# Optimization experiments

Hardware: AMD Instinct MI355X
Metric: run time of the kernel (lower is better)

## Reference

```python
import jax, jax.numpy as jnp
import numpy as np

N_NODES = 100000
N_EDGES = 1600000
IN_C = 128
HID = 128
OUT_C = 10
N_GRAPHS = 512


def setup_inputs() -> dict:
    key = jax.random.key(0)
    ks = jax.random.split(key, 12)
    x = jax.random.normal(ks[0], (N_NODES, IN_C), dtype=jnp.float32)
    edge_index = jax.random.randint(ks[1], (2, N_EDGES), 0, N_NODES, dtype=jnp.int64)
    batch = jnp.sort(jax.random.randint(ks[2], (N_NODES,), 0, N_GRAPHS, dtype=jnp.int64))

    def lin(k, fan_in, fan_out):
        bound = 1.0 / np.sqrt(fan_in)
        return jax.random.uniform(k, (fan_in, fan_out), jnp.float32, -bound, bound)

    params = {
        # GraphConv layer i: W_rel (neighbor aggregate transform, with bias),
        # W_root (self transform, no bias) -- matches PyG GraphConv.
        "W1_rel": lin(ks[3], IN_C, HID), "b1": jnp.zeros((HID,), jnp.float32), "W1_root": lin(ks[4], IN_C, HID),
        "W2_rel": lin(ks[5], HID, HID), "b2": jnp.zeros((HID,), jnp.float32), "W2_root": lin(ks[6], HID, HID),
        "W3_rel": lin(ks[7], HID, HID), "b3": jnp.zeros((HID,), jnp.float32), "W3_root": lin(ks[8], HID, HID),
        "W_lin": lin(ks[9], HID, OUT_C), "b_lin": jnp.zeros((OUT_C,), jnp.float32),
    }
    return {"x": x, "edge_index": edge_index, "batch": batch, **params}


def _graph_conv(x, src, dst, W_rel, b, W_root):
    # PyG GraphConv with aggr='add': out_i = W_rel @ sum_{j->i} x_j + b + W_root @ x_i
    agg = jax.ops.segment_sum(x[src], dst, num_segments=x.shape[0])  # [N, d]
    return agg @ W_rel + b + x @ W_root


def reference(x, edge_index, batch,
              W1_rel, b1, W1_root,
              W2_rel, b2, W2_root,
              W3_rel, b3, W3_root,
              W_lin, b_lin):
    src, dst = edge_index[0], edge_index[1]
    h = jax.nn.relu(_graph_conv(x, src, dst, W1_rel, b1, W1_root))
    h = jax.nn.relu(_graph_conv(h, src, dst, W2_rel, b2, W2_root))
    h = _graph_conv(h, src, dst, W3_rel, b3, W3_root)
    # global mean pool over graphs
    sums = jax.ops.segment_sum(h, batch, num_segments=N_GRAPHS)             # [G, d]
    counts = jax.ops.segment_sum(jnp.ones((h.shape[0],), h.dtype), batch, num_segments=N_GRAPHS)
    pooled = sums / jnp.maximum(counts, 1.0)[:, None]
    return pooled @ W_lin + b_lin  # [G, OUT_C]
```

## Files before the change

### kernel.cpp

```cpp
#include <hip/hip_runtime.h>

static constexpr int NN = 100000;
static constexpr int NE = 1600000;
static constexpr int C  = 128;
static constexpr int OC = 10;
static constexpr int NG = 512;

static constexpr int BSH  = 9;
static constexpr int BNW  = 1 << BSH;
static constexpr int BK   = (NN + BNW - 1) / BNW;
static constexpr int BCAP = 12288;
static constexpr int EPB  = 8192;
static constexpr int ABLK = (NE + EPB - 1) / EPB;

static constexpr int TSTRIDE = 132;
static constexpr int NSPLIT = 8;

typedef unsigned short u16;
typedef __attribute__((ext_vector_type(8))) short short8;
typedef __attribute__((ext_vector_type(8))) short bf16x8;
typedef __attribute__((ext_vector_type(4))) float f32x4;

__device__ __forceinline__ float bf2f(u16 u) {
    union { float f; unsigned int u32; } v; v.u32 = ((unsigned int)u) << 16; return v.f;
}
__device__ __forceinline__ u16 f2bf(float f) {
    union { float f; unsigned int u; } v; v.f = f;
    unsigned int u = v.u;
    unsigned int r = u + 0x7FFF + ((u >> 16) & 1);
    return (u16)(r >> 16);
}

__global__ __launch_bounds__(256) void k_binA(const int* __restrict__ src,
                                              const int* __restrict__ dst,
                                              int* __restrict__ gcnt,
                                              int* __restrict__ buck) {
    __shared__ int cnt[BK];
    __shared__ int curs[BK];
    int tid = threadIdx.x;
    for (int i = tid; i < BK; i += 256) cnt[i] = 0;
    __syncthreads();
    int e0 = blockIdx.x * EPB;
    for (int i = tid; i < EPB; i += 256) {
        int e = e0 + i;
        if (e < NE) atomicAdd(&cnt[dst[e] >> BSH], 1);
    }
    __syncthreads();
    for (int i = tid; i < BK; i += 256) {
        int c = cnt[i];
        int gb = (c > 0) ? atomicAdd(&gcnt[i], c) : 0;
        curs[i] = i * BCAP + gb;
    }
    __syncthreads();
    for (int i = tid; i < EPB; i += 256) {
        int e = e0 + i;
        if (e < NE) {
            int d = dst[e];
            int b = d >> BSH;
            int p = atomicAdd(&curs[b], 1);
            if (p < (b + 1) * BCAP)
                buck[p] = (src[e] << BSH) | (d & (BNW - 1));
        }
    }
}

__global__ __launch_bounds__(256) void k_meta(const int* __restrict__ gcnt,
                                              int* __restrict__ csrbase,
                                              int* __restrict__ rp,
                                              const int* __restrict__ batch,
                                              int* __restrict__ gstart) {
    int tid = threadIdx.x;
    if (blockIdx.x == 0) {
        __shared__ int buf[256];
        int v = (tid < BK) ? gcnt[tid] : 0;
        buf[tid] = v;
        __syncthreads();
        for (int off = 1; off < 256; off <<= 1) {
            int t = (tid >= off) ? buf[tid - off] : 0;
            __syncthreads();
            buf[tid] += t;
            __syncthreads();
        }
        if (tid < BK) csrbase[tid] = buf[tid] - v;
        if (tid == 0) rp[NN] = NE;
    } else {
        int g = (blockIdx.x - 1) * 256 + tid;
        if (g > NG) return;
        int lo = 0, hi = NN;
        while (lo < hi) { int mid = (lo + hi) >> 1; if (batch[mid] < g) lo = mid + 1; else hi = mid; }
        gstart[g] = lo;
    }
}

__global__ __launch_bounds__(BNW) void k_binB(const int* __restrict__ gcnt,
                                              const int* __restrict__ csrbase,
                                              const int* __restrict__ buck,
                                              int* __restrict__ rp,
                                              int* __restrict__ csr) {
    int b = blockIdx.x;
    int tid = threadIdx.x;
    __shared__ int hist[BNW];
    __shared__ int scanbuf[BNW];
    int n = gcnt[b];
    if (n > BCAP) n = BCAP;
    int base = csrbase[b];
    const int* bb = buck + (size_t)b * BCAP;

    hist[tid] = 0;
    __syncthreads();
    for (int i = tid; i < n; i += BNW) atomicAdd(&hist[bb[i] & (BNW - 1)], 1);
    __syncthreads();

    int v = hist[tid];
    scanbuf[tid] = v;
    __syncthreads();
    for (int off = 1; off < BNW; off <<= 1) {
        int t = (tid >= off) ? scanbuf[tid - off] : 0;
        __syncthreads();
        scanbuf[tid] += t;
        __syncthreads();
    }
    int excl = scanbuf[tid] - v;
    int node = (b << BSH) + tid;
    if (node < NN) rp[node] = base + excl;
    __syncthreads();
    hist[tid] = base + excl;
    __syncthreads();
    for (int i = tid; i < n; i += BNW) {
        int en = bb[i];
        int p = atomicAdd(&hist[en & (BNW - 1)], 1);
        csr[p] = en >> BSH;
    }
}

__global__ __launch_bounds__(256) void k_prep(
    const float* __restrict__ x, u16* __restrict__ xb,
    const float* __restrict__ W1r, const float* __restrict__ W1o,
    const float* __restrict__ W2r, const float* __restrict__ W2o,
    u16* __restrict__ Bp) {
    int bid = blockIdx.x;
    if (bid < 32) {
        int layer = bid >> 4;
        const float* Wr = (layer == 0) ? W1r : W2r;
        const float* Wo = (layer == 0) ? W1o : W2o;
        u16* out = Bp + layer * 32768;
        int t = (bid & 15) * 256 + threadIdx.x;
        int lane = t & 63;
        int nfrag = (t >> 6) & 7;
        int kk = t >> 9;
        int col = nfrag * 16 + (lane & 15);
        int k0 = kk * 32 + (lane >> 4) * 8;
        u16 vals[8];
#pragma unroll
        for (int j = 0; j < 8; ++j) {
            int k = k0 + j;
            float w = (k < C) ? Wr[k * C + col] : Wo[(k - C) * C + col];
            vals[j] = f2bf(w);
        }
        *reinterpret_cast<short8*>(out + (size_t)t * 8) = *reinterpret_cast<const short8*>(vals);
    } else {
        int i = (bid - 32) * 256 + threadIdx.x;
        size_t base = (size_t)i * 8;
        if (base >= (size_t)NN * C) return;
        float4 a = *reinterpret_cast<const float4*>(x + base);
        float4 b = *reinterpret_cast<const float4*>(x + base + 4);
        u16 o[8] = { f2bf(a.x), f2bf(a.y), f2bf(a.z), f2bf(a.w),
                     f2bf(b.x), f2bf(b.y), f2bf(b.z), f2bf(b.w) };
        *reinterpret_cast<short8*>(xb + base) = *reinterpret_cast<const short8*>(o);
    }
}

__global__ __launch_bounds__(256) void k_wfold(
    const float* __restrict__ W3r, const float* __restrict__ W3o,
    const float* __restrict__ b3, const float* __restrict__ W_lin,
    const float* __restrict__ b_lin,
    float* __restrict__ Wrl, float* __restrict__ Wro, float* __restrict__ bfold) {
    int o = blockIdx.x;
    int tid = threadIdx.x;
    if (tid < 128) {
        float s = 0.0f;
#pragma unroll 8
        for (int c = 0; c < C; ++c) s += W3r[tid * C + c] * W_lin[c * OC + o];
        Wrl[tid * OC + o] = s;
    } else {
        int k = tid - 128;
        float s = 0.0f;
#pragma unroll 8
        for (int c = 0; c < C; ++c) s += W3o[k * C + c] * W_lin[c * OC + o];
        Wro[k * OC + o] = s;
    }
    if (tid == 0) {
        float s = 0.0f;
        for (int c = 0; c < C; ++c) s += b3[c] * W_lin[c * OC + o];
        bfold[o] = b_lin[o] + s;
    }
}

__global__ __launch_bounds__(256) void k_gather(const u16* __restrict__ h,
                                                const int* __restrict__ rp,
                                                const int* __restrict__ csr,
                                                u16* __restrict__ agg) {
    int t = blockIdx.x * blockDim.x + threadIdx.x;
    int node = t >> 6;
    if (node >= NN) return;
    int lane = t & 63;
    int jj = lane >> 4;
    int seg = (lane & 15) * 8;
    int beg = rp[node], end = rp[node + 1];

    float acc[8] = {};
    int j0 = beg;
    for (; j0 + 8 <= end; j0 += 8) {
        int sa = csr[j0 + jj];
        int sb = csr[j0 + 4 + jj];
        short8 va = *reinterpret_cast<const short8*>(h + (size_t)sa * C + seg);
        short8 vb = *reinterpret_cast<const short8*>(h + (size_t)sb * C + seg);
#pragma unroll
        for (int q = 0; q < 8; ++q) {
            acc[q] += bf2f((u16)va[q]);
            acc[q] += bf2f((u16)vb[q]);
        }
    }
    if (j0 < end) {
        int ja = j0 + jj;
        int jb = j0 + 4 + jj;
        if (ja < end) {
            int sa = csr[ja];
            short8 va = *reinterpret_cast<const short8*>(h + (size_t)sa * C + seg);
#pragma unroll
            for (int q = 0; q < 8; ++q) acc[q] += bf2f((u16)va[q]);
        }
        if (jb < end) {
            int sb = csr[jb];
            short8 vb = *reinterpret_cast<const short8*>(h + (size_t)sb * C + seg);
#pragma unroll
            for (int q = 0; q < 8; ++q) acc[q] += bf2f((u16)vb[q]);
        }
    }

#pragma unroll
    for (int q = 0; q < 8; ++q) {
        acc[q] += __shfl_xor(acc[q], 32);
        acc[q] += __shfl_xor(acc[q], 16);
    }
    if (lane < 16) {
        u16 o[8];
#pragma unroll
        for (int q = 0; q < 8; ++q) o[q] = f2bf(acc[q]);
        *reinterpret_cast<short8*>(agg + (size_t)node * C + seg) =
            *reinterpret_cast<const short8*>(o);
    }
}

template <bool RELU>
__global__ __launch_bounds__(256) void k_transform_mfma(
    const u16* __restrict__ agg, const u16* __restrict__ h,
    const u16* __restrict__ Bp, const float* __restrict__ bias,
    u16* __restrict__ out) {
    __shared__ u16 tile[4][16 * TSTRIDE];
    int wave = threadIdx.x >> 6;
    int lane = threadIdx.x & 63;
    int row0 = blockIdx.x * 64 + wave * 16;
    int arow = row0 + (lane & 15);
    int rclamp = arow < NN ? arow : NN - 1;
    int koff = (lane >> 4) * 8;

    f32x4 acc[8] = {};
#pragma unroll
    for (int kk = 0; kk < 8; ++kk) {
        bf16x8 a;
        if (kk < 4) {
            a = *reinterpret_cast<const bf16x8*>(agg + (size_t)rclamp * C + kk * 32 + koff);
        } else {
            a = *reinterpret_cast<const bf16x8*>(h + (size_t)rclamp * C + (kk - 4) * 32 + koff);
        }
        const u16* bp = Bp + ((size_t)kk * 8 * 64 + lane) * 8;
#pragma unroll
        for (int n = 0; n < 8; ++n) {
            bf16x8 b = *reinterpret_cast<const bf16x8*>(bp + (size_t)n * 64 * 8);
            acc[n] = __builtin_amdgcn_mfma_f32_16x16x32_bf16(a, b, acc[n], 0, 0, 0);
        }
    }

    u16* T = tile[wave];
    int colbase = lane & 15;
    int rloc = (lane >> 4) * 4;
#pragma unroll
    for (int n = 0; n < 8; ++n) {
        int col = n * 16 + colbase;
        float bb = bias[col];
#pragma unroll
        for (int r = 0; r < 4; ++r) {
            float v = acc[n][r] + bb;
            if (RELU) v = fmaxf(v, 0.0f);
            T[(rloc + r) * TSTRIDE + col] = f2bf(v);
        }
    }
    __syncthreads();

#pragma unroll
    for (int k = 0; k < 4; ++k) {
        int idx = k * 64 + lane;
        int lr = idx >> 4;
        int off = (idx & 15) * 8;
        int ro = row0 + lr;
        if (ro < NN) {
            short8 v = *reinterpret_cast<const short8*>(&T[lr * TSTRIDE + off]);
            *reinterpret_cast<short8*>(out + (size_t)ro * C + off) = v;
        }
    }
}

__global__ __launch_bounds__(256) void k_gsum(
    const u16* __restrict__ h, const int* __restrict__ rp,
    const int* __restrict__ csr, const int* __restrict__ gstart,
    float* __restrict__ partial) {
    int b = blockIdx.x;
    int g = b >> 3;
    int p = b & 7;
    int slot = threadIdx.x >> 4;
    int seg = (threadIdx.x & 15) * 8;

    int gs = gstart[g], ge = gstart[g + 1];
    int es = rp[gs], ee = rp[ge];
    int m = ee - es;
    int js = es + (int)(((long long)m * p) >> 3);
    int je = es + (int)(((long long)m * (p + 1)) >> 3);
    int nn = ge - gs;
    int is = gs + (int)(((long long)nn * p) >> 3);
    int ie = gs + (int)(((long long)nn * (p + 1)) >> 3);

    float accS[8] = {};
    int j = js + slot;
    for (; j + 16 < je; j += 32) {
        int r0 = csr[j];
        int r1 = csr[j + 16];
        short8 v0 = *reinterpret_cast<const short8*>(h + (size_t)r0 * C + seg);
        short8 v1 = *reinterpret_cast<const short8*>(h + (size_t)r1 * C + seg);
#pragma unroll
        for (int q = 0; q < 8; ++q) {
            accS[q] += bf2f((u16)v0[q]);
            accS[q] += bf2f((u16)v1[q]);
        }
    }
    if (j < je) {
        int r0 = csr[j];
        short8 v0 = *reinterpret_cast<const short8*>(h + (size_t)r0 * C + seg);
#pragma unroll
        for (int q = 0; q < 8; ++q) accS[q] += bf2f((u16)v0[q]);
    }

    float accT[8] = {};
    for (int i = is + slot; i < ie; i += 16) {
        short8 v = *reinterpret_cast<const short8*>(h + (size_t)i * C + seg);
#pragma unroll
        for (int q = 0; q < 8; ++q) accT[q] += bf2f((u16)v[q]);
    }

    __shared__ float red[16][C];
#pragma unroll
    for (int q = 0; q < 8; ++q) red[slot][seg + q] = accS[q];
    __syncthreads();
    if (threadIdx.x < C) {
        float s = 0.0f;
#pragma unroll
        for (int r = 0; r < 16; ++r) s += red[r][threadIdx.x];
        partial[(size_t)b * 256 + threadIdx.x] = s;
    }
    __syncthreads();
#pragma unroll
    for (int q = 0; q < 8; ++q) red[slot][seg + q] = accT[q];
    __syncthreads();
    if (threadIdx.x < C) {
        float s = 0.0f;
#pragma unroll
        for (int r = 0; r < 16; ++r) s += red[r][threadIdx.x];
        partial[(size_t)b * 256 + 128 + threadIdx.x] = s;
    }
}

__global__ __launch_bounds__(128) void k_gout(
    const float* __restrict__ partial, const int* __restrict__ gstart,
    const float* __restrict__ Wrl, const float* __restrict__ Wro,
    const float* __restrict__ bfold, float* __restrict__ out) {
    int g = blockIdx.x;
    int k = threadIdx.x;
    __shared__ float S[C], T[C];
    float s = 0.0f, t = 0.0f;
#pragma unroll
    for (int p = 0; p < NSPLIT; ++p) {
        s += partial[((size_t)(g * NSPLIT + p)) * 256 + k];
        t += partial[((size_t)(g * NSPLIT + p)) * 256 + 128 + k];
    }
    S[k] = s;
    T[k] = t;
    __syncthreads();
    if (k < OC) {
        int n = gstart[g + 1] - gstart[g];
        float inv = 1.0f / (float)max(n, 1);
        float o = bfold[k];
#pragma unroll 8
        for (int kk = 0; kk < C; ++kk)
            o += (S[kk] * Wrl[kk * OC + k] + T[kk] * Wro[kk * OC + k]) * inv;
        out[g * OC + k] = o;
    }
}

extern "C" void kernel_launch(void* const* d_in, const int* in_sizes, int n_in,
                              void* d_out, int out_size, void* d_ws, size_t ws_size,
                              hipStream_t stream) {
    const float* x       = (const float*)d_in[0];
    const int*   eidx    = (const int*)d_in[1];
    const int*   batch   = (const int*)d_in[2];
    const float* W1_rel  = (const float*)d_in[3];
    const float* b1      = (const float*)d_in[4];
    const float* W1_root = (const float*)d_in[5];
    const float* W2_rel  = (const float*)d_in[6];
    const float* b2      = (const float*)d_in[7];
    const float* W2_root = (const float*)d_in[8];
    const float* W3_rel  = (const float*)d_in[9];
    const float* b3      = (const float*)d_in[10];
    const float* W3_root = (const float*)d_in[11];
    const float* W_lin   = (const float*)d_in[12];
    const float* b_lin   = (const float*)d_in[13];
    float* out = (float*)d_out;

    const int* src = eidx;
    const int* dst = eidx + NE;

    u16* xb   = (u16*)d_ws;
    u16* hb   = xb + (size_t)NN * C;
    u16* aggb = hb + (size_t)NN * C;
    u16* Bp   = aggb + (size_t)NN * C;
    int* rp      = (int*)(Bp + 2 * 32768);
    int* csr     = rp + NN + 1;
    int* buck    = csr + NE;
    int* gcnt    = buck + (size_t)BK * BCAP;
    int* csrbase = gcnt + BK;
    int* gstart  = csrbase + BK;
    float* partial = (float*)(gstart + NG + 2);
    float* Wrl   = partial + (size_t)NG * NSPLIT * 256;
    float* Wro   = Wrl + C * OC;
    float* bfold = Wro + C * OC;

    const int gb = (NN * 64 + 255) / 256;
    const int tb = (NN + 63) / 64;
    const int prepb = 32 + ((NN * C / 8) + 255) / 256;

    hipMemsetAsync(gcnt, 0, BK * sizeof(int), stream);
    k_binA<<<ABLK, 256, 0, stream>>>(src, dst, gcnt, buck);
    k_meta<<<4, 256, 0, stream>>>(gcnt, csrbase, rp, batch, gstart);
    k_binB<<<BK, BNW, 0, stream>>>(gcnt, csrbase, buck, rp, csr);

    k_prep<<<prepb, 256, 0, stream>>>(x, xb, W1_rel, W1_root, W2_rel, W2_root, Bp);
    k_wfold<<<OC, 256, 0, stream>>>(W3_rel, W3_root, b3, W_lin, b_lin, Wrl, Wro, bfold);

    k_gather<<<gb, 256, 0, stream>>>(xb, rp, csr, aggb);
    k_transform_mfma<true><<<tb, 256, 0, stream>>>(aggb, xb, Bp, b1, hb);

    k_gather<<<gb, 256, 0, stream>>>(hb, rp, csr, aggb);
    k_transform_mfma<true><<<tb, 256, 0, stream>>>(aggb, hb, Bp + 32768, b2, hb);

    k_gsum<<<NG * NSPLIT, 256, 0, stream>>>(hb, rp, csr, gstart, partial);
    k_gout<<<NG, 128, 0, stream>>>(partial, gstart, Wrl, Wro, bfold, out);
}
```

Before: 317.3 us.

## Fold meta scan into binB, merge wfold into prep, fuse root pooling into transform

```diff
diff --git a/kernel.cpp b/kernel.cpp
--- a/kernel.cpp
+++ b/kernel.cpp
@@ -10,7 +10,7 @@
 static constexpr int BNW  = 1 << BSH;
 static constexpr int BK   = (NN + BNW - 1) / BNW;
 static constexpr int BCAP = 12288;
-static constexpr int EPB  = 8192;
+static constexpr int EPB  = 4096;
 static constexpr int ABLK = (NE + EPB - 1) / EPB;
 
 static constexpr int TSTRIDE = 132;
@@ -64,36 +64,7 @@
     }
 }
 
-__global__ __launch_bounds__(256) void k_meta(const int* __restrict__ gcnt,
-                                              int* __restrict__ csrbase,
-                                              int* __restrict__ rp,
-                                              const int* __restrict__ batch,
-                                              int* __restrict__ gstart) {
-    int tid = threadIdx.x;
-    if (blockIdx.x == 0) {
-        __shared__ int buf[256];
-        int v = (tid < BK) ? gcnt[tid] : 0;
-        buf[tid] = v;
-        __syncthreads();
-        for (int off = 1; off < 256; off <<= 1) {
-            int t = (tid >= off) ? buf[tid - off] : 0;
-            __syncthreads();
-            buf[tid] += t;
-            __syncthreads();
-        }
-        if (tid < BK) csrbase[tid] = buf[tid] - v;
-        if (tid == 0) rp[NN] = NE;
-    } else {
-        int g = (blockIdx.x - 1) * 256 + tid;
-        if (g > NG) return;
-        int lo = 0, hi = NN;
-        while (lo < hi) { int mid = (lo + hi) >> 1; if (batch[mid] < g) lo = mid + 1; else hi = mid; }
-        gstart[g] = lo;
-    }
-}
-
 __global__ __launch_bounds__(BNW) void k_binB(const int* __restrict__ gcnt,
-                                              const int* __restrict__ csrbase,
                                               const int* __restrict__ buck,
                                               int* __restrict__ rp,
                                               int* __restrict__ csr) {
@@ -101,18 +72,8 @@
     int tid = threadIdx.x;
     __shared__ int hist[BNW];
     __shared__ int scanbuf[BNW];
-    int n = gcnt[b];
-    if (n > BCAP) n = BCAP;
-    int base = csrbase[b];
-    const int* bb = buck + (size_t)b * BCAP;
-
-    hist[tid] = 0;
-    __syncthreads();
-    for (int i = tid; i < n; i += BNW) atomicAdd(&hist[bb[i] & (BNW - 1)], 1);
-    __syncthreads();
-
-    int v = hist[tid];
-    scanbuf[tid] = v;
+
+    scanbuf[tid] = (tid < b) ? gcnt[tid] : 0;
     __syncthreads();
     for (int off = 1; off < BNW; off <<= 1) {
         int t = (tid >= off) ? scanbuf[tid - off] : 0;
@@ -120,9 +81,30 @@
         scanbuf[tid] += t;
         __syncthreads();
     }
+    int base = scanbuf[BNW - 1];
+
+    int n = gcnt[b];
+    if (n > BCAP) n = BCAP;
+    const int* bb = buck + (size_t)b * BCAP;
+
+    hist[tid] = 0;
+    __syncthreads();
+    for (int i = tid; i < n; i += BNW) atomicAdd(&hist[bb[i] & (BNW - 1)], 1);
+    __syncthreads();
+
+    int v = hist[tid];
+    scanbuf[tid] = v;
+    __syncthreads();
+    for (int off = 1; off < BNW; off <<= 1) {
+        int t = (tid >= off) ? scanbuf[tid - off] : 0;
+        __syncthreads();
+        scanbuf[tid] += t;
+        __syncthreads();
+    }
     int excl = scanbuf[tid] - v;
     int node = (b << BSH) + tid;
     if (node < NN) rp[node] = base + excl;
+    if (b == 0 && tid == 0) rp[NN] = NE;
     __syncthreads();
     hist[tid] = base + excl;
     __syncthreads();
@@ -137,14 +119,20 @@
     const float* __restrict__ x, u16* __restrict__ xb,
     const float* __restrict__ W1r, const float* __restrict__ W1o,
     const float* __restrict__ W2r, const float* __restrict__ W2o,
-    u16* __restrict__ Bp) {
+    u16* __restrict__ Bp,
+    const int* __restrict__ batch, int* __restrict__ gstart,
+    const float* __restrict__ W3r, const float* __restrict__ W3o,
+    const float* __restrict__ b3, const float* __restrict__ W_lin,
+    const float* __restrict__ b_lin,
+    float* __restrict__ Wrl, float* __restrict__ Wro, float* __restrict__ bfold) {
     int bid = blockIdx.x;
+    int tid = threadIdx.x;
     if (bid < 32) {
         int layer = bid >> 4;
         const float* Wr = (layer == 0) ? W1r : W2r;
         const float* Wo = (layer == 0) ? W1o : W2o;
-        u16* out = Bp + layer * 32768;
-        int t = (bid & 15) * 256 + threadIdx.x;
+        u16* outp = Bp + layer * 32768;
+        int t = (bid & 15) * 256 + tid;
         int lane = t & 63;
         int nfrag = (t >> 6) & 7;
         int kk = t >> 9;
@@ -157,9 +145,34 @@
             float w = (k < C) ? Wr[k * C + col] : Wo[(k - C) * C + col];
             vals[j] = f2bf(w);
         }
-        *reinterpret_cast<short8*>(out + (size_t)t * 8) = *reinterpret_cast<const short8*>(vals);
+        *reinterpret_cast<short8*>(outp + (size_t)t * 8) = *reinterpret_cast<const short8*>(vals);
+    } else if (bid < 35) {
+        int g = (bid - 32) * 256 + tid;
+        if (g > NG) return;
+        int lo = 0, hi = NN;
+        while (lo < hi) { int mid = (lo + hi) >> 1; if (batch[mid] < g) lo = mid + 1; else hi = mid; }
+        gstart[g] = lo;
+    } else if (bid < 45) {
+        int o = bid - 35;
+        if (tid < 128) {
+            float s = 0.0f;
+#pragma unroll 8
+            for (int c = 0; c < C; ++c) s += W3r[tid * C + c] * W_lin[c * OC + o];
+            Wrl[tid * OC + o] = s;
+        } else {
+            int k = tid - 128;
+            float s = 0.0f;
+#pragma unroll 8
+            for (int c = 0; c < C; ++c) s += W3o[k * C + c] * W_lin[c * OC + o];
+            Wro[k * OC + o] = s;
+        }
+        if (tid == 0) {
+            float s = 0.0f;
+            for (int c = 0; c < C; ++c) s += b3[c] * W_lin[c * OC + o];
+            bfold[o] = b_lin[o] + s;
+        }
     } else {
-        int i = (bid - 32) * 256 + threadIdx.x;
+        int i = (bid - 45) * 256 + tid;
         size_t base = (size_t)i * 8;
         if (base >= (size_t)NN * C) return;
         float4 a = *reinterpret_cast<const float4*>(x + base);
@@ -167,32 +180,6 @@
         u16 o[8] = { f2bf(a.x), f2bf(a.y), f2bf(a.z), f2bf(a.w),
                      f2bf(b.x), f2bf(b.y), f2bf(b.z), f2bf(b.w) };
         *reinterpret_cast<short8*>(xb + base) = *reinterpret_cast<const short8*>(o);
-    }
-}
-
-__global__ __launch_bounds__(256) void k_wfold(
-    const float* __restrict__ W3r, const float* __restrict__ W3o,
-    const float* __restrict__ b3, const float* __restrict__ W_lin,
-    const float* __restrict__ b_lin,
-    float* __restrict__ Wrl, float* __restrict__ Wro, float* __restrict__ bfold) {
-    int o = blockIdx.x;
-    int tid = threadIdx.x;
-    if (tid < 128) {
-        float s = 0.0f;
-#pragma unroll 8
-        for (int c = 0; c < C; ++c) s += W3r[tid * C + c] * W_lin[c * OC + o];
-        Wrl[tid * OC + o] = s;
-    } else {
-        int k = tid - 128;
-        float s = 0.0f;
-#pragma unroll 8
-        for (int c = 0; c < C; ++c) s += W3o[k * C + c] * W_lin[c * OC + o];
-        Wro[k * OC + o] = s;
-    }
-    if (tid == 0) {
-        float s = 0.0f;
-        for (int c = 0; c < C; ++c) s += b3[c] * W_lin[c * OC + o];
-        bfold[o] = b_lin[o] + s;
     }
 }
 
@@ -252,11 +239,12 @@
     }
 }
 
-template <bool RELU>
+template <bool RELU, bool TSUM>
 __global__ __launch_bounds__(256) void k_transform_mfma(
     const u16* __restrict__ agg, const u16* __restrict__ h,
     const u16* __restrict__ Bp, const float* __restrict__ bias,
-    u16* __restrict__ out) {
+    u16* __restrict__ out,
+    const int* __restrict__ batch, float* __restrict__ Tpart) {
     __shared__ u16 tile[4][16 * TSTRIDE];
     int wave = threadIdx.x >> 6;
     int lane = threadIdx.x & 63;
@@ -307,6 +295,27 @@
         if (ro < NN) {
             short8 v = *reinterpret_cast<const short8*>(&T[lr * TSTRIDE + off]);
             *reinterpret_cast<short8*>(out + (size_t)ro * C + off) = v;
+        }
+    }
+
+    if (TSUM) {
+        if (threadIdx.x < C) {
+            int c = threadIdx.x;
+            int base = blockIdx.x * 64;
+            float run = 0.0f;
+            int curg = -1;
+            for (int r = 0; r < 64; ++r) {
+                int ro = base + r;
+                if (ro >= NN) break;
+                int g = batch[ro];
+                if (g != curg) {
+                    if (curg >= 0) atomicAdd(&Tpart[(size_t)curg * C + c], run);
+                    run = 0.0f;
+                    curg = g;
+                }
+                run += bf2f(tile[r >> 4][(r & 15) * TSTRIDE + c]);
+            }
+            if (curg >= 0) atomicAdd(&Tpart[(size_t)curg * C + c], run);
         }
     }
 }
@@ -326,74 +335,59 @@
     int m = ee - es;
     int js = es + (int)(((long long)m * p) >> 3);
     int je = es + (int)(((long long)m * (p + 1)) >> 3);
-    int nn = ge - gs;
-    int is = gs + (int)(((long long)nn * p) >> 3);
-    int ie = gs + (int)(((long long)nn * (p + 1)) >> 3);
-
-    float accS[8] = {};
+
+    float acc[8] = {};
     int j = js + slot;
-    for (; j + 16 < je; j += 32) {
+    for (; j + 48 < je; j += 64) {
         int r0 = csr[j];
         int r1 = csr[j + 16];
+        int r2 = csr[j + 32];
+        int r3 = csr[j + 48];
         short8 v0 = *reinterpret_cast<const short8*>(h + (size_t)r0 * C + seg);
         short8 v1 = *reinterpret_cast<const short8*>(h + (size_t)r1 * C + seg);
+        short8 v2 = *reinterpret_cast<const short8*>(h + (size_t)r2 * C + seg);
+        short8 v3 = *reinterpret_cast<const short8*>(h + (size_t)r3 * C + seg);
 #pragma unroll
         for (int q = 0; q < 8; ++q) {
-            accS[q] += bf2f((u16)v0[q]);
-            accS[q] += bf2f((u16)v1[q]);
-        }
-    }
-    if (j < je) {
+            acc[q] += bf2f((u16)v0[q]);
+            acc[q] += bf2f((u16)v1[q]);
+            acc[q] += bf2f((u16)v2[q]);
+            acc[q] += bf2f((u16)v3[q]);
+        }
+    }
+    for (; j < je; j += 16) {
         int r0 = csr[j];
         short8 v0 = *reinterpret_cast<const short8*>(h + (size_t)r0 * C + seg);
 #pragma unroll
-        for (int q = 0; q < 8; ++q) accS[q] += bf2f((u16)v0[q]);
-    }
-
-    float accT[8] = {};
-    for (int i = is + slot; i < ie; i += 16) {
-        short8 v = *reinterpret_cast<const short8*>(h + (size_t)i * C + seg);
-#pragma unroll
-        for (int q = 0; q < 8; ++q) accT[q] += bf2f((u16)v[q]);
+        for (int q = 0; q < 8; ++q) acc[q] += bf2f((u16)v0[q]);
     }
 
     __shared__ float red[16][C];
 #pragma unroll
-    for (int q = 0; q < 8; ++q) red[slot][seg + q] = accS[q];
+    for (int q = 0; q < 8; ++q) red[slot][seg + q] = acc[q];
     __syncthreads();
     if (threadIdx.x < C) {
         float s = 0.0f;
 #pragma unroll
         for (int r = 0; r < 16; ++r) s += red[r][threadIdx.x];
-        partial[(size_t)b * 256 + threadIdx.x] = s;
-    }
-    __syncthreads();
-#pragma unroll
-    for (int q = 0; q < 8; ++q) red[slot][seg + q] = accT[q];
-    __syncthreads();
-    if (threadIdx.x < C) {
-        float s = 0.0f;
-#pragma unroll
-        for (int r = 0; r < 16; ++r) s += red[r][threadIdx.x];
-        partial[(size_t)b * 256 + 128 + threadIdx.x] = s;
+        partial[(size_t)b * C + threadIdx.x] = s;
     }
 }
 
 __global__ __launch_bounds__(128) void k_gout(
-    const float* __restrict__ partial, const int* __restrict__ gstart,
+    const float* __restrict__ partial, const float* __restrict__ Tpart,
+    const int* __restrict__ gstart,
     const float* __restrict__ Wrl, const float* __restrict__ Wro,
     const float* __restrict__ bfold, float* __restrict__ out) {
     int g = blockIdx.x;
     int k = threadIdx.x;
     __shared__ float S[C], T[C];
-    float s = 0.0f, t = 0.0f;
-#pragma unroll
-    for (int p = 0; p < NSPLIT; ++p) {
-        s += partial[((size_t)(g * NSPLIT + p)) * 256 + k];
-        t += partial[((size_t)(g * NSPLIT + p)) * 256 + 128 + k];
-    }
+    float s = 0.0f;
+#pragma unroll
+    for (int p = 0; p < NSPLIT; ++p)
+        s += partial[((size_t)(g * NSPLIT + p)) * C + k];
     S[k] = s;
-    T[k] = t;
+    T[k] = Tpart[(size_t)g * C + k];
     __syncthreads();
     if (k < OC) {
         int n = gstart[g + 1] - gstart[g];
@@ -436,31 +430,33 @@
     int* csr     = rp + NN + 1;
     int* buck    = csr + NE;
     int* gcnt    = buck + (size_t)BK * BCAP;
-    int* csrbase = gcnt + BK;
-    int* gstart  = csrbase + BK;
+    float* Tpart = (float*)(gcnt + BK);
+    int* gstart  = (int*)(Tpart + (size_t)NG * C);
     float* partial = (float*)(gstart + NG + 2);
-    float* Wrl   = partial + (size_t)NG * NSPLIT * 256;
+    float* Wrl   = partial + (size_t)NG * NSPLIT * C;
     float* Wro   = Wrl + C * OC;
     float* bfold = Wro + C * OC;
 
     const int gb = (NN * 64 + 255) / 256;
     const int tb = (NN + 63) / 64;
-    const int prepb = 32 + ((NN * C / 8) + 255) / 256;
-
-    hipMemsetAsync(gcnt, 0, BK * sizeof(int), stream);
+    const int prepb = 45 + ((NN * C / 8) + 255) / 256;
+
+    hipMemsetAsync(gcnt, 0, BK * sizeof(int) + (size_t)NG * C * sizeof(float), stream);
     k_binA<<<ABLK, 256, 0, stream>>>(src, dst, gcnt, buck);
-    k_meta<<<4, 256, 0, stream>>>(gcnt, csrbase, rp, batch, gstart);
-    k_binB<<<BK, BNW, 0, stream>>>(gcnt, csrbase, buck, rp, csr);
-
-    k_prep<<<prepb, 256, 0, stream>>>(x, xb, W1_rel, W1_root, W2_rel, W2_root, Bp);
-    k_wfold<<<OC, 256, 0, stream>>>(W3_rel, W3_root, b3, W_lin, b_lin, Wrl, Wro, bfold);
+    k_binB<<<BK, BNW, 0, stream>>>(gcnt, buck, rp, csr);
+
+    k_prep<<<prepb, 256, 0, stream>>>(x, xb, W1_rel, W1_root, W2_rel, W2_root, Bp,
+                                      batch, gstart, W3_rel, W3_root, b3, W_lin,
+                                      b_lin, Wrl, Wro, bfold);
 
     k_gather<<<gb, 256, 0, stream>>>(xb, rp, csr, aggb);
-    k_transform_mfma<true><<<tb, 256, 0, stream>>>(aggb, xb, Bp, b1, hb);
+    k_transform_mfma<true, false><<<tb, 256, 0, stream>>>(aggb, xb, Bp, b1, hb,
+                                                          batch, Tpart);
 
     k_gather<<<gb, 256, 0, stream>>>(hb, rp, csr, aggb);
-    k_transform_mfma<true><<<tb, 256, 0, stream>>>(aggb, hb, Bp + 32768, b2, hb);
+    k_transform_mfma<true, true><<<tb, 256, 0, stream>>>(aggb, hb, Bp + 32768, b2,
+                                                         hb, batch, Tpart);
 
     k_gsum<<<NG * NSPLIT, 256, 0, stream>>>(hb, rp, csr, gstart, partial);
-    k_gout<<<NG, 128, 0, stream>>>(partial, gstart, Wrl, Wro, bfold, out);
-}
+    k_gout<<<NG, 128, 0, stream>>>(partial, Tpart, gstart, Wrl, Wro, bfold, out);
+}
```

Measured after the change: 309.0 us. 2.6% less time.
